# Kernel tuning notes

Measured on AMD Instinct MI355X. Metric: run time of the kernel, lower is better.

## Reference

```python
import jax, jax.numpy as jnp
import numpy as np

B, N, M_PARAM, F_IN, HEADS, HID, OUT, MLP_H, N_ACT = 64, 512, 50, 3, 2, 3, 3, 128, 512
NEG_SLOPE = 0.2


def setup_inputs() -> dict:
    key = jax.random.key(0)
    ks = jax.random.split(key, 20)
    s = 0.1
    idx = jax.random.uniform(ks[0], (B, N), dtype=jnp.float32)
    x = jax.random.normal(ks[1], (B, N, F_IN), dtype=jnp.float32)
    y = jax.random.normal(ks[2], (B, M_PARAM + 2, F_IN), dtype=jnp.float32)
    adj = (jax.random.uniform(ks[3], (B, N, N)) < 0.02).astype(jnp.float32)
    # GATConv 1: in=3 -> heads=2, out=3 (concat)
    W1 = jax.random.normal(ks[4], (F_IN, HEADS * HID), dtype=jnp.float32) * s
    a_src1 = jax.random.normal(ks[5], (HEADS, HID), dtype=jnp.float32) * s
    a_dst1 = jax.random.normal(ks[6], (HEADS, HID), dtype=jnp.float32) * s
    b1 = jnp.zeros((HEADS * HID,), dtype=jnp.float32)
    # GATConv 2: in=6 -> heads=1, out=3
    W2 = jax.random.normal(ks[7], (HEADS * HID, OUT), dtype=jnp.float32) * s
    a_src2 = jax.random.normal(ks[8], (1, OUT), dtype=jnp.float32) * s
    a_dst2 = jax.random.normal(ks[9], (1, OUT), dtype=jnp.float32) * s
    b2 = jnp.zeros((OUT,), dtype=jnp.float32)
    fc_in = N + N * OUT + (M_PARAM + 2) * 3  # 2204
    Wf1 = jax.random.normal(ks[10], (fc_in, MLP_H), dtype=jnp.float32) * (1.0 / np.sqrt(fc_in))
    bf1 = jnp.zeros((MLP_H,), dtype=jnp.float32)
    Wf2 = jax.random.normal(ks[11], (MLP_H, N_ACT), dtype=jnp.float32) * (1.0 / np.sqrt(MLP_H))
    bf2 = jnp.zeros((N_ACT,), dtype=jnp.float32)
    return {"idx": idx, "x": x, "y": y, "adj": adj,
            "W1": W1, "a_src1": a_src1, "a_dst1": a_dst1, "b1": b1,
            "W2": W2, "a_src2": a_src2, "a_dst2": a_dst2, "b2": b2,
            "Wf1": Wf1, "bf1": bf1, "Wf2": Wf2, "bf2": bf2}


def gat_layer(x, adj, W, a_src, a_dst, bias):
    # PyG GATConv (concat=True): h = x W; alpha_ij = softmax_i(leaky_relu(a_src.h_i + a_dst.h_j))
    # edge (i -> j) exists iff adj[i, j] != 0; self-loops added per PyG default.
    Bb, Nn = x.shape[0], x.shape[1]
    Hh, D = a_src.shape
    h = (x @ W).reshape(Bb, Nn, Hh, D)                     # [B,N,H,D]
    es = jnp.einsum('bnhd,hd->bnh', h, a_src)              # source term
    ed = jnp.einsum('bnhd,hd->bnh', h, a_dst)              # target term
    logits = es[:, :, None, :] + ed[:, None, :, :]         # [B, i(src), j(dst), H]
    logits = jax.nn.leaky_relu(logits, NEG_SLOPE)
    mask = (adj > 0) | jnp.eye(Nn, dtype=bool)[None]       # self-loops
    logits = jnp.where(mask[..., None], logits, jnp.float32(-1e9))
    alpha = jax.nn.softmax(logits, axis=1)                 # softmax over sources per target
    out = jnp.einsum('bijh,bihd->bjhd', alpha, h)          # aggregate at targets
    return out.reshape(Bb, Nn, Hh * D) + bias


def reference(idx, x, y, adj, W1, a_src1, a_dst1, b1, W2, a_src2, a_dst2, b2, Wf1, bf1, Wf2, bf2):
    g = jax.nn.relu(gat_layer(x, adj, W1, a_src1, a_dst1, b1))
    g = gat_layer(g, adj, W2, a_src2, a_dst2, b2)          # heads=1
    feat = jnp.concatenate([idx.reshape(B, -1), g.reshape(B, -1), y.reshape(B, -1)], axis=-1)
    h = jax.nn.relu(feat @ Wf1 + bf1)
    return h @ Wf2 + bf2
```

## Files before the change

kernel.cpp:

```cpp
#include <hip/hip_runtime.h>
#include <hip/hip_bf16.h>
#include <stdint.h>

#define B_    64
#define N_    512
#define M2    52
#define MLPH  128
#define NACT  512
#define FC_IN 2204
#define NCH   18
#define NEG   0.2f
#define NW    16

__device__ __forceinline__ float lrelu(float v){ return v > 0.f ? v : NEG * v; }

__global__ __launch_bounds__(512) void kfuse1(const float* __restrict__ adj,
                                              const float* __restrict__ x,
                                              const float* __restrict__ W1,
                                              const float* __restrict__ as1,
                                              const float* __restrict__ ad1,
                                              const float* __restrict__ b1,
                                              const float* __restrict__ W2,
                                              const float* __restrict__ as2,
                                              uint32_t* __restrict__ maskT,
                                              float* __restrict__ node2){
  __shared__ uint32_t lm[2][64][16];
  __shared__ float node[N_][8];
  int b  = blockIdx.y;
  int j0 = blockIdx.x * 64;
  int t  = threadIdx.x;

  {
    int j4 = t & 15;
    int w  = (t >> 4) & 15;
    int kh = t >> 8;
    const float* basef = adj + ((size_t)(b * N_ + (w << 5) + (kh << 4))) * N_ + (j0 + (j4 << 2));
    uint32_t m0 = 0, m1 = 0, m2 = 0, m3 = 0;
#pragma unroll
    for (int k = 0; k < 16; ++k) {
      float4 v = *(const float4*)(basef + (size_t)k * N_);
      m0 |= (v.x > 0.f ? 1u : 0u) << k;
      m1 |= (v.y > 0.f ? 1u : 0u) << k;
      m2 |= (v.z > 0.f ? 1u : 0u) << k;
      m3 |= (v.w > 0.f ? 1u : 0u) << k;
    }
    int sh = kh << 4;
    lm[kh][(j4 << 2) + 0][w] = m0 << sh;
    lm[kh][(j4 << 2) + 1][w] = m1 << sh;
    lm[kh][(j4 << 2) + 2][w] = m2 << sh;
    lm[kh][(j4 << 2) + 3][w] = m3 << sh;
  }

  {
    float xv0 = x[((size_t)(b * N_ + t)) * 3 + 0];
    float xv1 = x[((size_t)(b * N_ + t)) * 3 + 1];
    float xv2 = x[((size_t)(b * N_ + t)) * 3 + 2];
    float h[6];
#pragma unroll
    for (int c = 0; c < 6; ++c) h[c] = xv0 * W1[c] + xv1 * W1[6 + c] + xv2 * W1[12 + c];
#pragma unroll
    for (int c = 0; c < 6; ++c) node[t][c] = h[c];
    node[t][6] = h[0] * as1[0] + h[1] * as1[1] + h[2] * as1[2];
    node[t][7] = h[3] * as1[3] + h[4] * as1[4] + h[5] * as1[5];
  }
  __syncthreads();

  int w  = t & 15;
  int tg = t >> 4;
  float ad10 = ad1[0], ad11 = ad1[1], ad12 = ad1[2];
  float ad13 = ad1[3], ad14 = ad1[4], ad15 = ad1[5];
  float b10 = b1[0], b11 = b1[1], b12 = b1[2], b13 = b1[3], b14 = b1[4], b15 = b1[5];
  float as20 = as2[0], as21 = as2[1], as22 = as2[2];

#pragma unroll
  for (int p = 0; p < 2; ++p) {
    int jj = tg + p * 32;
    int j  = j0 + jj;
    uint32_t bits = lm[0][jj][w] | lm[1][jj][w];
    maskT[((size_t)(b * N_ + j)) * NW + w] = bits;
    if ((j >> 5) == w) bits |= 1u << (j & 31);

    float ed0 = node[j][0] * ad10 + node[j][1] * ad11 + node[j][2] * ad12;
    float ed1 = node[j][3] * ad13 + node[j][4] * ad14 + node[j][5] * ad15;

    float den0 = 0.f, den1 = 0.f;
    float a0 = 0.f, a1 = 0.f, a2 = 0.f, a3 = 0.f, a4 = 0.f, a5 = 0.f;
    while (bits) {
      int k = __ffs(bits) - 1;
      bits &= bits - 1;
      int i = (w << 5) + k;
      float e0 = __expf(lrelu(node[i][6] + ed0));
      float e1 = __expf(lrelu(node[i][7] + ed1));
      den0 += e0; den1 += e1;
      a0 += e0 * node[i][0]; a1 += e0 * node[i][1]; a2 += e0 * node[i][2];
      a3 += e1 * node[i][3]; a4 += e1 * node[i][4]; a5 += e1 * node[i][5];
    }
#pragma unroll
    for (int m = 1; m < 16; m <<= 1) {
      den0 += __shfl_xor(den0, m); den1 += __shfl_xor(den1, m);
      a0 += __shfl_xor(a0, m); a1 += __shfl_xor(a1, m); a2 += __shfl_xor(a2, m);
      a3 += __shfl_xor(a3, m); a4 += __shfl_xor(a4, m); a5 += __shfl_xor(a5, m);
    }
    float r0 = 1.f / den0, r1 = 1.f / den1;
    float g0 = fmaxf(a0 * r0 + b10, 0.f);
    float g1v = fmaxf(a1 * r0 + b11, 0.f);
    float g2v = fmaxf(a2 * r0 + b12, 0.f);
    float g3 = fmaxf(a3 * r1 + b13, 0.f);
    float g4 = fmaxf(a4 * r1 + b14, 0.f);
    float g5 = fmaxf(a5 * r1 + b15, 0.f);
    float h20 = g0*W2[0] + g1v*W2[3] + g2v*W2[6] + g3*W2[9]  + g4*W2[12] + g5*W2[15];
    float h21 = g0*W2[1] + g1v*W2[4] + g2v*W2[7] + g3*W2[10] + g4*W2[13] + g5*W2[16];
    float h22 = g0*W2[2] + g1v*W2[5] + g2v*W2[8] + g3*W2[11] + g4*W2[14] + g5*W2[17];
    float es2 = h20 * as20 + h21 * as21 + h22 * as22;
    if (w < 4) {
      float outv = (w == 0) ? h20 : (w == 1) ? h21 : (w == 2) ? h22 : es2;
      node2[((size_t)(b * N_ + j)) * 4 + w] = outv;
    }
  }
}

__global__ __launch_bounds__(256) void kagg2(const float* __restrict__ node2,
                                             const float* __restrict__ ad2,
                                             const float* __restrict__ b2,
                                             const uint32_t* __restrict__ maskT,
                                             float* __restrict__ g2){
  __shared__ float sn[N_][4];
  int b = blockIdx.y, tile = blockIdx.x, t = threadIdx.x;

  const float4* src = (const float4*)(node2 + (size_t)b * N_ * 4);
  for (int e = t; e < N_; e += 256) {
    float4 v = src[e];
    sn[e][0] = v.x; sn[e][1] = v.y; sn[e][2] = v.z; sn[e][3] = v.w;
  }
  __syncthreads();

  int w = t & 15, tg = t >> 4;
  int j = tile * 16 + tg;
  float ad20 = ad2[0], ad21 = ad2[1], ad22 = ad2[2];

  uint32_t bits = maskT[((size_t)(b * N_ + j)) * NW + w];
  if ((j >> 5) == w) bits |= 1u << (j & 31);

  float ed = sn[j][0] * ad20 + sn[j][1] * ad21 + sn[j][2] * ad22;
  float den = 0.f, a0 = 0.f, a1 = 0.f, a2 = 0.f;
  while (bits) {
    int k = __ffs(bits) - 1;
    bits &= bits - 1;
    int i = (w << 5) + k;
    float e = __expf(lrelu(sn[i][3] + ed));
    den += e;
    a0 += e * sn[i][0]; a1 += e * sn[i][1]; a2 += e * sn[i][2];
  }
#pragma unroll
  for (int m = 1; m < 16; m <<= 1) {
    den += __shfl_xor(den, m);
    a0 += __shfl_xor(a0, m); a1 += __shfl_xor(a1, m); a2 += __shfl_xor(a2, m);
  }
  if (w < 3) {
    float r = 1.f / den;
    float v = (w == 0 ? a0 : w == 1 ? a1 : a2) * r + b2[w];
    g2[((size_t)(b * N_ + j)) * 3 + w] = v;
  }
}

__global__ __launch_bounds__(256) void kmlp1v(const float* __restrict__ idx,
                                              const float* __restrict__ y,
                                              const float* __restrict__ g2,
                                              const float* __restrict__ Wf1,
                                              float* __restrict__ partial){
  __shared__ float fs[128];
  __shared__ float pr[8][128];
  int c = blockIdx.x, b = blockIdx.y, t = threadIdx.x;
  if (t < 128) {
    int k = c * 128 + t;
    float v = 0.f;
    if (k < N_)            v = idx[(size_t)b * N_ + k];
    else if (k < 2048)     v = g2[(size_t)b * (N_ * 3) + (k - N_)];
    else if (k < FC_IN)    v = y[(size_t)b * (M2 * 3) + (k - 2048)];
    fs[t] = v;
  }
  __syncthreads();

  int kq = t >> 5, ug = t & 31;
  int klen = min(128, FC_IN - c * 128);
  int kend = klen - kq * 16;
  const float4* wrow = (const float4*)(Wf1 + ((size_t)(c * 128 + kq * 16)) * MLPH) + ug;
  float a0 = 0.f, a1 = 0.f, a2 = 0.f, a3 = 0.f;
#pragma unroll
  for (int k2 = 0; k2 < 16; ++k2) {
    if (k2 < kend) {
      float fv = fs[kq * 16 + k2];
      float4 w = wrow[k2 * 32];
      a0 += fv * w.x; a1 += fv * w.y; a2 += fv * w.z; a3 += fv * w.w;
    }
  }
  *(float4*)&pr[kq][ug * 4] = make_float4(a0, a1, a2, a3);
  __syncthreads();
  if (t < 128) {
    float s = 0.f;
#pragma unroll
    for (int q = 0; q < 8; ++q) s += pr[q][t];
    partial[((size_t)b * NCH + c) * MLPH + t] = s;
  }
}

__global__ __launch_bounds__(256) void kmlp2v(const float* __restrict__ partial,
                                              const float* __restrict__ bf1,
                                              const float* __restrict__ Wf2,
                                              const float* __restrict__ bf2,
                                              float* __restrict__ out){
  __shared__ float part[NCH * MLPH];
  __shared__ float hid[MLPH];
  __shared__ float pr[8][128];
  int q = blockIdx.x, b = blockIdx.y, t = threadIdx.x;

  const float4* src = (const float4*)(partial + (size_t)b * NCH * MLPH);
  float4* dst = (float4*)part;
  for (int e = t; e < (NCH * MLPH) / 4; e += 256) dst[e] = src[e];
  __syncthreads();
  if (t < 128) {
    float s = bf1[t];
#pragma unroll
    for (int c2 = 0; c2 < NCH; ++c2) s += part[c2 * MLPH + t];
    hid[t] = fmaxf(s, 0.f);
  }
  __syncthreads();

  int kh = t >> 5, ug = t & 31;
  const float4* wrow = (const float4*)(Wf2 + (size_t)(kh * 16) * NACT + q * 128) + ug;
  float a0 = 0.f, a1 = 0.f, a2 = 0.f, a3 = 0.f;
#pragma unroll
  for (int k2 = 0; k2 < 16; ++k2) {
    float hv = hid[kh * 16 + k2];
    float4 w = wrow[k2 * 128];
    a0 += hv * w.x; a1 += hv * w.y; a2 += hv * w.z; a3 += hv * w.w;
  }
  *(float4*)&pr[kh][ug * 4] = make_float4(a0, a1, a2, a3);
  __syncthreads();
  if (t < 128) {
    float s = bf2[q * 128 + t];
#pragma unroll
    for (int h = 0; h < 8; ++h) s += pr[h][t];
    out[(size_t)b * NACT + q * 128 + t] = s;
  }
}

extern "C" void kernel_launch(void* const* d_in, const int* in_sizes, int n_in,
                              void* d_out, int out_size, void* d_ws, size_t ws_size,
                              hipStream_t stream) {
  const float* idx = (const float*)d_in[0];
  const float* x   = (const float*)d_in[1];
  const float* y   = (const float*)d_in[2];
  const float* adj = (const float*)d_in[3];
  const float* W1  = (const float*)d_in[4];
  const float* as1 = (const float*)d_in[5];
  const float* ad1 = (const float*)d_in[6];
  const float* b1  = (const float*)d_in[7];
  const float* W2  = (const float*)d_in[8];
  const float* as2 = (const float*)d_in[9];
  const float* ad2 = (const float*)d_in[10];
  const float* b2  = (const float*)d_in[11];
  const float* Wf1 = (const float*)d_in[12];
  const float* bf1 = (const float*)d_in[13];
  const float* Wf2 = (const float*)d_in[14];
  const float* bf2 = (const float*)d_in[15];
  float* out = (float*)d_out;

  uint8_t* ws = (uint8_t*)d_ws;
  uint32_t* maskT = (uint32_t*)ws;
  float* node2    = (float*)(ws + 2097152);
  float* g2       = (float*)(ws + 2097152 + 524288);
  float* partial  = (float*)(ws + 2097152 + 524288 + 393216);

  hipLaunchKernelGGL(kfuse1, dim3(8, B_),   dim3(512), 0, stream,
                     adj, x, W1, as1, ad1, b1, W2, as2, maskT, node2);
  hipLaunchKernelGGL(kagg2,  dim3(32, B_),  dim3(256), 0, stream,
                     node2, ad2, b2, maskT, g2);
  hipLaunchKernelGGL(kmlp1v, dim3(NCH, B_), dim3(256), 0, stream,
                     idx, y, g2, Wf1, partial);
  hipLaunchKernelGGL(kmlp2v, dim3(4, B_),   dim3(256), 0, stream,
                     partial, bf1, Wf2, bf2, out);
}
```

Before: 35.32 us.

## Process 128 targets per kagg2 block and stage mask tile in LDS

kagg2 now launches 4 blocks per batch instead of 32, and each block covers 128 target nodes in 8 rounds. The node2 table is staged into shared memory once per 128 targets rather than once per 16, which cuts redundant global loads, and the block's mask rows are preloaded into LDS with vectorized loads. kmlp1v specializes the full-chunk path so the per-iteration bound check goes away, and kmlp2v unrolls its shared-memory copy. The cost is fewer blocks (256 total), which lowers parallelism and gives longer serial work per thread.

```diff
diff --git a/kernel.cpp b/kernel.cpp
--- a/kernel.cpp
+++ b/kernel.cpp
@@ -125,41 +125,50 @@
                                              const uint32_t* __restrict__ maskT,
                                              float* __restrict__ g2){
   __shared__ float sn[N_][4];
-  int b = blockIdx.y, tile = blockIdx.x, t = threadIdx.x;
-
-  const float4* src = (const float4*)(node2 + (size_t)b * N_ * 4);
-  for (int e = t; e < N_; e += 256) {
-    float4 v = src[e];
-    sn[e][0] = v.x; sn[e][1] = v.y; sn[e][2] = v.z; sn[e][3] = v.w;
-  }
-  __syncthreads();
-
-  int w = t & 15, tg = t >> 4;
-  int j = tile * 16 + tg;
+  __shared__ uint32_t smq[128][NW];
+  int q = blockIdx.x, b = blockIdx.y, t = threadIdx.x;
+
+  const float4* nsrc = (const float4*)(node2 + (size_t)b * N_ * 4);
+  const uint4*  msrc = (const uint4*)(maskT + ((size_t)b * N_ + q * 128) * NW);
+  float4 nv0 = nsrc[t];
+  float4 nv1 = nsrc[t + 256];
+  uint4  mv0 = msrc[t];
+  uint4  mv1 = msrc[t + 256];
+  sn[t][0] = nv0.x; sn[t][1] = nv0.y; sn[t][2] = nv0.z; sn[t][3] = nv0.w;
+  sn[t + 256][0] = nv1.x; sn[t + 256][1] = nv1.y; sn[t + 256][2] = nv1.z; sn[t + 256][3] = nv1.w;
+  ((uint4*)smq)[t] = mv0;
+  ((uint4*)smq)[t + 256] = mv1;
+  __syncthreads();
+
+  int w = t & 15, grp = t >> 4;
   float ad20 = ad2[0], ad21 = ad2[1], ad22 = ad2[2];
-
-  uint32_t bits = maskT[((size_t)(b * N_ + j)) * NW + w];
-  if ((j >> 5) == w) bits |= 1u << (j & 31);
-
-  float ed = sn[j][0] * ad20 + sn[j][1] * ad21 + sn[j][2] * ad22;
-  float den = 0.f, a0 = 0.f, a1 = 0.f, a2 = 0.f;
-  while (bits) {
-    int k = __ffs(bits) - 1;
-    bits &= bits - 1;
-    int i = (w << 5) + k;
-    float e = __expf(lrelu(sn[i][3] + ed));
-    den += e;
-    a0 += e * sn[i][0]; a1 += e * sn[i][1]; a2 += e * sn[i][2];
-  }
-#pragma unroll
-  for (int m = 1; m < 16; m <<= 1) {
-    den += __shfl_xor(den, m);
-    a0 += __shfl_xor(a0, m); a1 += __shfl_xor(a1, m); a2 += __shfl_xor(a2, m);
-  }
-  if (w < 3) {
-    float r = 1.f / den;
-    float v = (w == 0 ? a0 : w == 1 ? a1 : a2) * r + b2[w];
-    g2[((size_t)(b * N_ + j)) * 3 + w] = v;
+  float b20 = b2[0], b21 = b2[1], b22 = b2[2];
+#pragma unroll
+  for (int r = 0; r < 8; ++r) {
+    int jl = r * 16 + grp;
+    int j  = q * 128 + jl;
+    uint32_t bits = smq[jl][w];
+    if ((j >> 5) == w) bits |= 1u << (j & 31);
+    float ed = sn[j][0] * ad20 + sn[j][1] * ad21 + sn[j][2] * ad22;
+    float den = 0.f, a0 = 0.f, a1 = 0.f, a2 = 0.f;
+    while (bits) {
+      int k = __ffs(bits) - 1;
+      bits &= bits - 1;
+      int i = (w << 5) + k;
+      float e = __expf(lrelu(sn[i][3] + ed));
+      den += e;
+      a0 += e * sn[i][0]; a1 += e * sn[i][1]; a2 += e * sn[i][2];
+    }
+#pragma unroll
+    for (int m = 1; m < 16; m <<= 1) {
+      den += __shfl_xor(den, m);
+      a0 += __shfl_xor(a0, m); a1 += __shfl_xor(a1, m); a2 += __shfl_xor(a2, m);
+    }
+    if (w < 3) {
+      float rr = 1.f / den;
+      float v = (w == 0 ? a0 : w == 1 ? a1 : a2) * rr + (w == 0 ? b20 : w == 1 ? b21 : b22);
+      g2[((size_t)(b * N_ + j)) * 3 + w] = v;
+    }
   }
 }
 
@@ -182,13 +191,18 @@
   __syncthreads();
 
   int kq = t >> 5, ug = t & 31;
-  int klen = min(128, FC_IN - c * 128);
-  int kend = klen - kq * 16;
   const float4* wrow = (const float4*)(Wf1 + ((size_t)(c * 128 + kq * 16)) * MLPH) + ug;
   float a0 = 0.f, a1 = 0.f, a2 = 0.f, a3 = 0.f;
-#pragma unroll
-  for (int k2 = 0; k2 < 16; ++k2) {
-    if (k2 < kend) {
+  if (c < 17) {
+#pragma unroll
+    for (int k2 = 0; k2 < 16; ++k2) {
+      float fv = fs[kq * 16 + k2];
+      float4 w = wrow[k2 * 32];
+      a0 += fv * w.x; a1 += fv * w.y; a2 += fv * w.z; a3 += fv * w.w;
+    }
+  } else {
+    int kend = min(16, (FC_IN - 17 * 128) - kq * 16);
+    for (int k2 = 0; k2 < kend; ++k2) {
       float fv = fs[kq * 16 + k2];
       float4 w = wrow[k2 * 32];
       a0 += fv * w.x; a1 += fv * w.y; a2 += fv * w.z; a3 += fv * w.w;
@@ -215,8 +229,12 @@
   int q = blockIdx.x, b = blockIdx.y, t = threadIdx.x;
 
   const float4* src = (const float4*)(partial + (size_t)b * NCH * MLPH);
-  float4* dst = (float4*)part;
-  for (int e = t; e < (NCH * MLPH) / 4; e += 256) dst[e] = src[e];
+  float4 v0 = src[t];
+  float4 v1 = src[t + 256];
+  float4 v2 = (t < 64) ? src[t + 512] : make_float4(0.f, 0.f, 0.f, 0.f);
+  ((float4*)part)[t] = v0;
+  ((float4*)part)[t + 256] = v1;
+  if (t < 64) ((float4*)part)[t + 512] = v2;
   __syncthreads();
   if (t < 128) {
     float s = bf1[t];
@@ -274,7 +292,7 @@
 
   hipLaunchKernelGGL(kfuse1, dim3(8, B_),   dim3(512), 0, stream,
                      adj, x, W1, as1, ad1, b1, W2, as2, maskT, node2);
-  hipLaunchKernelGGL(kagg2,  dim3(32, B_),  dim3(256), 0, stream,
+  hipLaunchKernelGGL(kagg2,  dim3(4, B_),   dim3(256), 0, stream,
                      node2, ad2, b2, maskT, g2);
   hipLaunchKernelGGL(kmlp1v, dim3(NCH, B_), dim3(256), 0, stream,
                      idx, y, g2, Wf1, partial);
```

Result: no change. 35.18 us (-0.4%).
